# Kernel optimization log

Measured on AMD Instinct MI355X. Metric: run time of the kernel, lower is better.

## Reference

```python
import jax, jax.numpy as jnp
import numpy as np

D, H, K, L, NB = 128, 8, 16, 16, 2
N, E, MN, ME = 100_000, 800_000, 1_000, 8_000
VOCAB, BT, VP = 50_000, 256, 15
_SQD, _SQK = float(np.sqrt(D)), float(np.sqrt(K))


def _segment_softmax(score, seg, num):
    m = jax.ops.segment_max(score, seg, num_segments=num)
    e = jnp.exp(score - m[seg])
    z = jax.ops.segment_sum(e, seg, num_segments=num)
    return e / (z[seg] + 1e-9)


def _meta_learner(feat, u, W2, W1):
    # latent-attention factorization: feat [n,D] -> 2d param [n,H,K], 1d param [n,H]
    w = jax.nn.softmax((feat @ u.T) / _SQD, axis=-1)  # [n,L]
    return jnp.einsum('nl,lhk->nhk', w, W2), w @ W1


def _conv(feat, src, dst, p2n, p1n, p2e, p1e, Wq, Wk, Wv, Wo):
    # HeteroAttnConv: multi-head attention message passing modulated by
    # per-node (p2n,p1n) and per-edge (p2e,p1e) meta parameters.
    n = feat.shape[0]
    q = (feat @ Wq).reshape(n, H, K) * p2n
    kf = (feat @ Wk).reshape(n, H, K)
    v = (feat @ Wv).reshape(n, H, K)
    ke = kf[src] * p2e                                   # [e,H,K]
    score = (q[dst] * ke).sum(-1) / _SQK + p1e + p1n[dst]  # [e,H]
    attn = _segment_softmax(score, dst, n)
    agg = jax.ops.segment_sum(attn[..., None] * v[src], dst, num_segments=n).reshape(n, D)
    return jax.nn.relu(agg @ Wo), ke.reshape(-1, D)


def _forward(emb, u, W2lat, W1lat, Wq_m, Wk_m, Wv_m, Wo_m, Wq, Wk, Wv, Wo,
             node_vals, meta_node_vals, src, dst, meta_src, meta_dst,
             meta_node_id, meta_edge_id, target_idx,
             static_vals, static_src, static_dst):
    # _init_meta_param: static param-name graph, copy_u/sum then meta_learner
    fs = emb[static_vals]
    agg = jax.ops.segment_sum(fs[static_src], static_dst, num_segments=VP)
    p2s, p1s = _meta_learner(agg, u, W2lat, W1lat)
    base_tw, base_n1, base_n2 = p1s[0], p1s[3], p2s[6]   # target_weight, node 1d, node 2d
    base_e1, base_e2 = p1s[9], p2s[12]                   # edge 1d, edge 2d

    meta_feat = emb[meta_node_vals]
    feat = emb[node_vals]
    # _asign_param_to_graph(meta_graph): broadcast base buffers only
    mp2n = jnp.broadcast_to(base_n2, (MN, H, K))
    mp1n = jnp.broadcast_to(base_n1, (MN, H))
    mp2e = jnp.broadcast_to(base_e2, (ME, H, K))
    mp1e = jnp.broadcast_to(base_e1, (ME, H))

    out = jnp.zeros((BT, 1), feat.dtype)
    for b in range(NB):
        pre_meta, pre = meta_feat, feat
        meta_feat, meta_edge_feat = _conv(meta_feat, meta_src, meta_dst,
                                          mp2n, mp1n, mp2e, mp1e,
                                          Wq_m[b], Wk_m[b], Wv_m[b], Wo_m[b])
        # _asign_param_to_graph(graph, meta_node_feat, meta_edge_feat):
        # base repeat + indexed add of meta_learner outputs
        p2mn, p1mn = _meta_learner(meta_feat, u, W2lat, W1lat)
        p2me, p1me = _meta_learner(meta_edge_feat, u, W2lat, W1lat)
        p2n = base_n2[None] + p2mn[meta_node_id]
        p1n = base_n1[None] + p1mn[meta_node_id]
        tw = base_tw[None] + p1mn[meta_node_id]
        p2e = base_e2[None] + p2me[meta_edge_id]
        p1e = base_e1[None] + p1me[meta_edge_id]
        feat, _ = _conv(feat, src, dst, p2n, p1n, p2e, p1e,
                        Wq[b], Wk[b], Wv[b], Wo[b])
        # block residual
        meta_feat = meta_feat + pre_meta
        feat = feat + pre
        # Target: per-target-node weighted readout with target_weight param
        logit = jnp.einsum('th,thk->t', tw[target_idx],
                           feat[target_idx].reshape(BT, H, K))
        out = out + logit[:, None]
    return out / NB


def setup_inputs() -> dict:
    key = jax.random.key(0)
    ks = jax.random.split(key, 24)
    s = 0.05
    inp = {}
    inp['emb'] = jax.random.normal(ks[0], (VOCAB, D), jnp.float32) * s
    inp['u'] = jax.random.normal(ks[1], (L, D), jnp.float32) * s
    inp['W2lat'] = jax.random.normal(ks[2], (L, H, K), jnp.float32) * s
    inp['W1lat'] = jax.random.normal(ks[3], (L, H), jnp.float32) * s
    for i, nm in enumerate(['Wq_m', 'Wk_m', 'Wv_m', 'Wo_m', 'Wq', 'Wk', 'Wv', 'Wo']):
        inp[nm] = jax.random.normal(ks[4 + i], (NB, D, D), jnp.float32) / np.sqrt(D)
    inp['node_vals'] = jax.random.randint(ks[12], (N,), 0, VOCAB)
    inp['meta_node_vals'] = jax.random.randint(ks[13], (MN,), 0, VOCAB)
    inp['src'] = jax.random.randint(ks[14], (E,), 0, N)
    inp['dst'] = jax.random.randint(ks[15], (E,), 0, N)
    inp['meta_src'] = jax.random.randint(ks[16], (ME,), 0, MN)
    inp['meta_dst'] = jax.random.randint(ks[17], (ME,), 0, MN)
    inp['meta_node_id'] = jax.random.randint(ks[18], (N,), 0, MN)
    inp['meta_edge_id'] = jax.random.randint(ks[19], (E,), 0, ME)
    inp['target_idx'] = jax.random.randint(ks[20], (BT,), 0, N)
    # static param-name graph: 5 names x (1 name node + 2 token nodes), tokens->name
    name_pos = np.arange(5) * 3
    inp['static_vals'] = jax.random.randint(ks[21], (VP,), 0, VOCAB)
    inp['static_src'] = jnp.asarray(np.stack([name_pos + 1, name_pos + 2], 1).reshape(-1), jnp.int32)
    inp['static_dst'] = jnp.asarray(np.repeat(name_pos, 2), jnp.int32)
    return inp


def reference(emb, u, W2lat, W1lat, Wq_m, Wk_m, Wv_m, Wo_m, Wq, Wk, Wv, Wo,
              node_vals, meta_node_vals, src, dst, meta_src, meta_dst,
              meta_node_id, meta_edge_id, target_idx,
              static_vals, static_src, static_dst):
    return _forward(emb, u, W2lat, W1lat, Wq_m, Wk_m, Wv_m, Wo_m, Wq, Wk, Wv, Wo,
                    node_vals, meta_node_vals, src, dst, meta_src, meta_dst,
                    meta_node_id, meta_edge_id, target_idx,
                    static_vals, static_src, static_dst)
```

## Files before the change

kernel.cpp:

```cpp
#include <hip/hip_runtime.h>
#include <hip/hip_bf16.h>
#include <hip/hip_fp8.h>

#define DD   128
#define HH   8

typedef short bf16x8 __attribute__((ext_vector_type(8)));
typedef float f32x4  __attribute__((ext_vector_type(4)));
typedef float f32x2  __attribute__((ext_vector_type(2)));

__device__ __forceinline__ float b2f(unsigned short v){
  union { unsigned int u; float f; } x; x.u = ((unsigned int)v) << 16; return x.f;
}
__device__ __forceinline__ unsigned short f2b(float f){
  __hip_bfloat16 h = __float2bfloat16(f);
  return *(unsigned short*)&h;
}
__device__ __forceinline__ unsigned char f2f8(float x){
  __hip_fp8_e4m3 h(x);
  return h.__x;
}
__device__ __forceinline__ float f82f(unsigned char b){
  __hip_fp8_e4m3 h; h.__x = b;
  return (float)h;
}
__device__ __forceinline__ void cvt4(unsigned int w, float* o){
#if defined(__has_builtin)
# if __has_builtin(__builtin_amdgcn_cvt_pk_f32_fp8)
  f32x2 lo = __builtin_amdgcn_cvt_pk_f32_fp8((int)w, false);
  f32x2 hi = __builtin_amdgcn_cvt_pk_f32_fp8((int)w, true);
  o[0]=lo[0]; o[1]=lo[1]; o[2]=hi[0]; o[3]=hi[1];
  return;
# endif
#endif
  o[0]=f82f(w&0xff); o[1]=f82f((w>>8)&0xff);
  o[2]=f82f((w>>16)&0xff); o[3]=f82f((w>>24)&0xff);
}
struct __align__(8) us4 { unsigned short x,y,z,w; };
struct __align__(16) us8 { unsigned short s[8]; };

__device__ __forceinline__ float gld(const void* p, size_t i, bool f32){
  if (f32) return ((const float*)p)[i];
  return b2f(((const unsigned short*)p)[i]);
}

__device__ __forceinline__ void gll16(const void* g, void* l){
  __builtin_amdgcn_global_load_lds(
      (const __attribute__((address_space(1))) unsigned int*)g,
      (__attribute__((address_space(3))) unsigned int*)l, 16, 0, 0);
}

struct WPtrs { const void* p[8]; };
__global__ __launch_bounds__(256) void w_repack16(
    WPtrs W, unsigned short* __restrict__ stage, int NBt,
    const int* __restrict__ dflag)
{
  const bool wf32 = (*dflag) != 0;
  int idx = blockIdx.x >> 6;
  int ti = idx / NBt, bi = idx - ti*NBt;
  size_t bo = (size_t)bi*DD*DD;
  int i = (blockIdx.x & 63)*256 + threadIdx.x;
  int k = i >> 7, n = i & 127;
  float x;
  if (wf32) x = ((const float*)W.p[ti])[bo + i];
  else      x = b2f(((const unsigned short*)W.p[ti])[bo + i]);
  stage[(size_t)idx*DD*DD + n*DD + k] = f2b(x);
}

enum { EPI_STORE=0, EPI_SCALE_CONST=1, EPI_RELU=3,
       EPI_RELU_RES=4, EPI_RELU_RES2=5 };

#define CPAD 132


template<int EPI, bool INB, bool OUTB>
__global__ __launch_bounds__(256) void gemm128m(
    const void* __restrict__ Av, const unsigned short* __restrict__ Bt,
    void* __restrict__ Cv, int M,
    const unsigned short* __restrict__ Rb,
    const float* __restrict__ Rf, float* __restrict__ C2)
{
  __shared__ __align__(16) unsigned short Asb[64*128];
  __shared__ __align__(16) unsigned short Btb[16896];
  const int tid = threadIdx.x;
  const int wave = tid >> 6, lane = tid & 63;
  const int row0 = blockIdx.x * 64;

  if (INB){
    const char* Ab = (const char*)Av;
    int n4 = lane >> 4, c = lane & 15;
#pragma unroll
    for (int op=0; op<4; op++){
      int rA = wave*16 + op*4;
      int n = rA + n4;
      int gr = row0 + n; if (gr >= M) gr = M - 1;
      gll16(Ab + (size_t)gr*256 + ((size_t)((c ^ (n & 7)) << 4)), &Asb[rA*128]);
    }
  } else {
    const float* Af = (const float*)Av;
    int r = tid >> 2, cb = (tid & 3) * 32, rx = (r & 7) << 3;
    int gr = row0 + r;
#pragma unroll
    for (int j=0;j<8;j++){
      int cc = cb + j*4;
      float4 val = make_float4(0.f,0.f,0.f,0.f);
      if (gr < M) val = *(const float4*)(Af + (size_t)gr*DD + cc);
      us4 o; o.x=f2b(val.x); o.y=f2b(val.y); o.z=f2b(val.z); o.w=f2b(val.w);
      *(us4*)&Asb[r*128 + (cc ^ rx)] = o;
    }
  }
  {
    int n4 = lane >> 4, c = lane & 15;
#pragma unroll
    for (int op=0; op<8; op++){
      int rB = wave*32 + op*4;
      int n = rB + n4;
      gll16((const char*)Bt + (size_t)n*256 + ((size_t)((c ^ (n & 7)) << 4)),
            &Btb[rB*128]);
    }
  }
  __syncthreads();

  f32x4 acc[8];
#pragma unroll
  for (int t=0;t<8;t++) acc[t] = (f32x4){0.f,0.f,0.f,0.f};
  const int am = (lane & 15), kq = (lane >> 4) * 8, axr = (am & 7) << 3;
#pragma unroll
  for (int k0=0;k0<128;k0+=32){
    int xo = (k0 + kq) ^ axr;
    bf16x8 a = *(bf16x8*)&Asb[(wave*16 + am)*128 + xo];
#pragma unroll
    for (int t=0;t<8;t++){
      bf16x8 b = *(bf16x8*)&Btb[(t*16 + am)*128 + xo];
      acc[t] = __builtin_amdgcn_mfma_f32_16x16x32_bf16(a, b, acc[t], 0,0,0);
    }
  }
  __syncthreads();
  float* Cls = (float*)Btb;
  {
    int rr = wave*16 + (lane>>4)*4;
    int cc = lane & 15;
#pragma unroll
    for (int t=0;t<8;t++)
#pragma unroll
      for (int r=0;r<4;r++)
        Cls[(rr + r)*CPAD + t*16 + cc] = acc[t][r];
  }
  __syncthreads();

  {
    int r = tid >> 2, cb = (tid & 3) * 32;
    int gr = row0 + r;
    if (gr < M){
#pragma unroll
      for (int j=0;j<8;j++){
        int c = cb + j*4;
        float4 o = *(float4*)&Cls[r*CPAD + c];
        if (EPI == EPI_RELU_RES){
          us4 rb = *(const us4*)(Rb + (size_t)gr*DD + c);
          o.x=fmaxf(o.x,0.f)+b2f(rb.x); o.y=fmaxf(o.y,0.f)+b2f(rb.y);
          o.z=fmaxf(o.z,0.f)+b2f(rb.z); o.w=fmaxf(o.w,0.f)+b2f(rb.w);
        } else if (EPI == EPI_RELU_RES2){
          o.x=fmaxf(o.x,0.f); o.y=fmaxf(o.y,0.f); o.z=fmaxf(o.z,0.f); o.w=fmaxf(o.w,0.f);
          float4 rf = *(const float4*)(Rf + (size_t)gr*DD + c);
          *(float4*)(C2 + (size_t)gr*DD + c) =
              make_float4(o.x+rf.x, o.y+rf.y, o.z+rf.z, o.w+rf.w);
        }
        if (OUTB){
          us4 ob; ob.x=f2b(o.x); ob.y=f2b(o.y); ob.z=f2b(o.z); ob.w=f2b(o.w);
          *(us4*)((unsigned short*)Cv + (size_t)gr*DD + c) = ob;
        } else {
          *(float4*)((float*)Cv + (size_t)gr*DD + c) = o;
        }
      }
    }
  }
}

template<int EPIQ, bool INB, bool FP8KV>
__device__ __forceinline__ void qkv_body(
    unsigned short* Asb, unsigned short* Btb, int blk,
    const void* __restrict__ Av,
    const unsigned short* __restrict__ Btq, const unsigned short* __restrict__ Btk,
    const unsigned short* __restrict__ Btv,
    void* __restrict__ Cq, void* __restrict__ Ck, int stK,
    void* __restrict__ Cvo, int stV, int M,
    const float* __restrict__ svec)
{
  const int tid = threadIdx.x;
  const int wave = tid >> 6, lane = tid & 63;
  const int row0 = blk * 64;

  if (INB){
    const char* Ab = (const char*)Av;
    int n4 = lane >> 4, c = lane & 15;
#pragma unroll
    for (int op=0; op<4; op++){
      int rA = wave*16 + op*4;
      int n = rA + n4;
      int gr = row0 + n; if (gr >= M) gr = M - 1;
      gll16(Ab + (size_t)gr*256 + ((size_t)((c ^ (n & 7)) << 4)), &Asb[rA*128]);
    }
  } else {
    const float* Af = (const float*)Av;
    int r = tid >> 2, cb = (tid & 3) * 32, rx = (r & 7) << 3;
    int gr = row0 + r;
#pragma unroll
    for (int j=0;j<8;j++){
      int cc = cb + j*4;
      float4 val = make_float4(0.f,0.f,0.f,0.f);
      if (gr < M) val = *(const float4*)(Af + (size_t)gr*DD + cc);
      us4 o; o.x=f2b(val.x); o.y=f2b(val.y); o.z=f2b(val.z); o.w=f2b(val.w);
      *(us4*)&Asb[r*128 + (cc ^ rx)] = o;
    }
  }

  const unsigned short* Bts[3] = {Btq, Btk, Btv};
  void* Cs[3] = {Cq, Ck, Cvo};
  const int sts[3] = {DD, stK, stV};
  const int am = (lane & 15), kq = (lane >> 4) * 8, axr = (am & 7) << 3;

  for (int ph=0; ph<3; ph++){
    {
      const unsigned short* Bt = Bts[ph];
      int n4 = lane >> 4, c = lane & 15;
#pragma unroll
      for (int op=0; op<8; op++){
        int rB = wave*32 + op*4;
        int n = rB + n4;
        gll16((const char*)Bt + (size_t)n*256 + ((size_t)((c ^ (n & 7)) << 4)),
              &Btb[rB*128]);
      }
    }
    __syncthreads();
    f32x4 acc[8];
#pragma unroll
    for (int t=0;t<8;t++) acc[t] = (f32x4){0.f,0.f,0.f,0.f};
#pragma unroll
    for (int k0=0;k0<128;k0+=32){
      int xo = (k0 + kq) ^ axr;
      bf16x8 a = *(bf16x8*)&Asb[(wave*16 + am)*128 + xo];
#pragma unroll
      for (int t=0;t<8;t++){
        bf16x8 b = *(bf16x8*)&Btb[(t*16 + am)*128 + xo];
        acc[t] = __builtin_amdgcn_mfma_f32_16x16x32_bf16(a, b, acc[t], 0,0,0);
      }
    }
    __syncthreads();
    float* Cls = (float*)Btb;
    {
      int rr = wave*16 + (lane>>4)*4;
      int cc = lane & 15;
#pragma unroll
      for (int t=0;t<8;t++)
#pragma unroll
        for (int r=0;r<4;r++)
          Cls[(rr + r)*CPAD + t*16 + cc] = acc[t][r];
    }
    __syncthreads();
    {
      int r = tid >> 2, cb = (tid & 3) * 32;
      int gr = row0 + r;
      if (gr < M){
#pragma unroll
        for (int j=0;j<8;j++){
          int c = cb + j*4;
          float4 o = *(float4*)&Cls[r*CPAD + c];
          if (ph == 0 && EPIQ == EPI_SCALE_CONST){
            o.x*=svec[c+0]; o.y*=svec[c+1]; o.z*=svec[c+2]; o.w*=svec[c+3];
          }
          if (FP8KV && ph > 0){
            unsigned char* Cb = (unsigned char*)Cs[ph];
            uchar4 ob;
            ob.x=f2f8(o.x*8.f); ob.y=f2f8(o.y*8.f);
            ob.z=f2f8(o.z*8.f); ob.w=f2f8(o.w*8.f);
            *(uchar4*)(Cb + (size_t)gr*256 + c) = ob;
          } else {
            us4 ob; ob.x=f2b(o.x); ob.y=f2b(o.y); ob.z=f2b(o.z); ob.w=f2b(o.w);
            *(us4*)((unsigned short*)Cs[ph] + (size_t)gr*sts[ph] + c) = ob;
          }
        }
      }
    }
    __syncthreads();
  }
}

__global__ __launch_bounds__(256) void gemm_qkv2(
    const unsigned short* __restrict__ featB, const float* __restrict__ featM,
    const unsigned short* __restrict__ wqb, const unsigned short* __restrict__ wkb,
    const unsigned short* __restrict__ wvb,
    const unsigned short* __restrict__ wqm, const unsigned short* __restrict__ wkm,
    const unsigned short* __restrict__ wvm,
    unsigned short* __restrict__ qB, unsigned char* __restrict__ kv8,
    unsigned short* __restrict__ qM, unsigned short* __restrict__ kfM,
    unsigned short* __restrict__ vM,
    int Nbig, int Nmeta, int gN, const float* __restrict__ svec)
{
  __shared__ __align__(16) unsigned short Asb[64*128];
  __shared__ __align__(16) unsigned short Btb[16896];
  if (blockIdx.x < gN){
    qkv_body<EPI_STORE,true,true>(Asb, Btb, blockIdx.x, featB,
        wqb, wkb, wvb, qB, kv8, 0, kv8 + 128, 0, Nbig, svec);
  } else {
    qkv_body<EPI_SCALE_CONST,false,false>(Asb, Btb, blockIdx.x - gN, featM,
        wqm, wkm, wvm, qM, kfM, DD, vM, DD, Nmeta, svec);
  }
}

__global__ __launch_bounds__(256) void k_static(
    const void* __restrict__ emb, const int* __restrict__ svals,
    const int* __restrict__ ssrc, const int* __restrict__ sdst,
    const void* __restrict__ u, const void* __restrict__ W2,
    const void* __restrict__ W1, float* __restrict__ base, int nsrc,
    int* __restrict__ dflag)
{
  __shared__ float sagg[15][128];
  __shared__ float ssc[15][16];
  __shared__ float sww[15][16];
  __shared__ int swf;
  const int t = threadIdx.x;
  if (t < 64){
    float m = 0.f;
    for (int i=t; i<128; i+=64){
      float x = fabsf(b2f(((const unsigned short*)emb)[i]));
      if (x < 1e30f) m = fmaxf(m, x);
    }
#pragma unroll
    for (int s=1;s<64;s<<=1) m = fmaxf(m, __shfl_xor(m, s, 64));
    if (t==0){ int f = (m > 1e4f) ? 1 : 0; *dflag = f; swf = f; }
  }
  for (int i=t;i<15*128;i+=256) ((float*)sagg)[i]=0.f;
  __syncthreads();
  const bool wf32 = (swf != 0);
  if (t < 128){
    for (int i=0;i<nsrc;i++){
      int row = sdst[i]; int vr = svals[ssrc[i]];
      sagg[row][t] += gld(emb, (size_t)vr*DD + t, wf32);
    }
  }
  __syncthreads();
  if (t < 240){
    int n = t>>4, l = t&15;
    float a=0.f;
    for (int d=0;d<128;d++) a += sagg[n][d]*gld(u, l*128+d, wf32);
    ssc[n][l] = a * 0.08838834764831845f;
  }
  __syncthreads();
  if (t < 15){
    float mx=-1e30f;
    for (int l=0;l<16;l++) mx = fmaxf(mx, ssc[t][l]);
    float s=0.f;
    for (int l=0;l<16;l++){ float e=__expf(ssc[t][l]-mx); sww[t][l]=e; s+=e; }
    float inv = 1.f/s;
    for (int l=0;l<16;l++) sww[t][l]*=inv;
  }
  __syncthreads();
  if (t < 8){
    float a=0.f,b=0.f,c=0.f;
    for (int l=0;l<16;l++){
      float wv = gld(W1, l*8+t, wf32);
      a += sww[0][l]*wv; b += sww[3][l]*wv; c += sww[9][l]*wv;
    }
    base[t]=a; base[8+t]=b; base[16+t]=c;
  }
  if (t < 128){
    float a=0.f,b=0.f;
    for (int l=0;l<16;l++){
      float wv = gld(W2, l*128+t, wf32);
      a += sww[6][l]*wv; b += sww[12][l]*wv;
    }
    base[24+t]=a; base[152+t]=b;
  }
}

__global__ __launch_bounds__(256) void gather_rows2(
    const void* __restrict__ emb,
    const int* __restrict__ valsB, unsigned short* __restrict__ featB, int nB,
    const int* __restrict__ valsM, float* __restrict__ featM, int nM,
    const int* __restrict__ dflag)
{
  const bool wf32 = (*dflag) != 0;
  int i = blockIdx.x*256 + threadIdx.x;
  bool big = (i < nB*16);
  int i2 = big ? i : (i - nB*16);
  if (!big && i2 >= nM*16) return;
  int r = i2>>4, c = (i2&15)*8;
  int vr = big ? valsB[r] : valsM[r];
  float vb[8];
  if (wf32){
    float4 f0 = *(const float4*)((const float*)emb + (size_t)vr*DD + c);
    float4 f1 = *(const float4*)((const float*)emb + (size_t)vr*DD + c + 4);
    vb[0]=f0.x; vb[1]=f0.y; vb[2]=f0.z; vb[3]=f0.w;
    vb[4]=f1.x; vb[5]=f1.y; vb[6]=f1.z; vb[7]=f1.w;
  } else {
    uint4 raw = *(const uint4*)((const unsigned short*)emb + (size_t)vr*DD + c);
    const unsigned short* hw = (const unsigned short*)&raw;
#pragma unroll
    for (int j=0;j<8;j++) vb[j] = b2f(hw[j]);
  }
  if (big){
    unsigned short* d = featB + (size_t)r*DD + c;
    us4 o0, o1;
    o0.x=f2b(vb[0]); o0.y=f2b(vb[1]); o0.z=f2b(vb[2]); o0.w=f2b(vb[3]);
    o1.x=f2b(vb[4]); o1.y=f2b(vb[5]); o1.z=f2b(vb[6]); o1.w=f2b(vb[7]);
    *(us4*)d = o0; *(us4*)(d+4) = o1;
  } else {
    float* d = featM + (size_t)r*DD + c;
    *(float4*)d     = make_float4(vb[0],vb[1],vb[2],vb[3]);
    *(float4*)(d+4) = make_float4(vb[4],vb[5],vb[6],vb[7]);
  }
}

__global__ __launch_bounds__(256) void zeroi(int* __restrict__ p, int n){
  int i = blockIdx.x*256 + threadIdx.x;
  if (i < n) p[i] = 0;
}

__global__ __launch_bounds__(256) void k_hist2(
    const int* __restrict__ dstB, const int* __restrict__ dstM,
    int* __restrict__ degB, int* __restrict__ degM, int E, int ME, int nbE){
  int b = blockIdx.x, t = threadIdx.x;
  if (b < nbE){ int i = b*256+t; if (i < E) atomicAdd(&degB[dstB[i]], 1); }
  else { int i = (b-nbE)*256+t; if (i < ME) atomicAdd(&degM[dstM[i]], 1); }
}

__global__ __launch_bounds__(256) void k_scan1b(
    const int* __restrict__ degB, int* __restrict__ rpB, int* __restrict__ bsB,
    int nB, int nbB,
    const int* __restrict__ degM, int* __restrict__ rpM, int* __restrict__ bsM,
    int nM){
  __shared__ int ls[256];
  int blk = blockIdx.x, t = threadIdx.x;
  const int* deg; int* rowptr; int* bsum; int n; int b;
  if (blk < nbB){ deg=degB; rowptr=rpB; bsum=bsB; n=nB; b=blk; }
  else          { deg=degM; rowptr=rpM; bsum=bsM; n=nM; b=blk-nbB; }
  int base = b*1024 + t*4;
  int v0 = (base+0<n)?deg[base+0]:0;
  int v1 = (base+1<n)?deg[base+1]:0;
  int v2 = (base+2<n)?deg[base+2]:0;
  int v3 = (base+3<n)?deg[base+3]:0;
  int tsum = v0+v1+v2+v3;
  ls[t] = tsum; __syncthreads();
  for (int o=1;o<256;o<<=1){
    int x = (t>=o) ? ls[t-o] : 0;
    __syncthreads();
    ls[t] += x;
    __syncthreads();
  }
  int excl = ls[t]-tsum;
  if (t==255) bsum[b] = ls[255];
  if (base+0<n) rowptr[base+0]=excl;
  if (base+1<n) rowptr[base+1]=excl+v0;
  if (base+2<n) rowptr[base+2]=excl+v0+v1;
  if (base+3<n) rowptr[base+3]=excl+v0+v1+v2;
}

__global__ __launch_bounds__(256) void k_scan3b(
    int* __restrict__ rpB, const int* __restrict__ bsB, int* __restrict__ curB,
    int nB, int nb3B, int nbsB,
    int* __restrict__ rpM, const int* __restrict__ bsM, int* __restrict__ curM,
    int nM, int nbsM){
  __shared__ int spre;
  int blk = blockIdx.x, t = threadIdx.x;
  if (blk < nb3B){
    if (t == 0){
      int chunk = blk >> 2;
      int pre = 0;
      for (int j=0;j<chunk;j++) pre += bsB[j];
      spre = pre;
      if (blk == 0){
        int tot = 0;
        for (int j=0;j<nbsB;j++) tot += bsB[j];
        rpB[nB] = tot;
      }
    }
    __syncthreads();
    int i = blk*256 + t;
    if (i < nB){ int r = rpB[i] + spre; rpB[i] = r; curB[i] = r; }
  } else {
    int b2 = blk - nb3B;
    if (t == 0){
      int chunk = b2 >> 2;
      int pre = 0;
      for (int j=0;j<chunk;j++) pre += bsM[j];
      spre = pre;
      if (b2 == 0){
        int tot = 0;
        for (int j=0;j<nbsM;j++) tot += bsM[j];
        rpM[nM] = tot;
      }
    }
    __syncthreads();
    int i = b2*256 + t;
    if (i < nM){ int r = rpM[i] + spre; rpM[i] = r; curM[i] = r; }
  }
}

__global__ __launch_bounds__(256) void k_scatter2(
    const int* __restrict__ dstB, const int* __restrict__ srcB,
    const int* __restrict__ auxB, int* __restrict__ curB,
    int* __restrict__ epackB, int E, int nbE,
    const int* __restrict__ dstM, const int* __restrict__ srcM,
    int* __restrict__ curM, int* __restrict__ esrcM, int* __restrict__ eauxM,
    int ME){
  int blk = blockIdx.x, t = threadIdx.x;
  if (blk < nbE){
    int e = blk*256 + t;
    if (e < E){
      int p = atomicAdd(&curB[dstB[e]], 1);
      epackB[p] = srcB[e] | (auxB[e] << 17);
    }
  } else {
    int e = (blk-nbE)*256 + t;
    if (e < ME){
      int p = atomicAdd(&curM[dstM[e]], 1);
      esrcM[p] = srcM[e];
      eauxM[p] = e;
    }
  }
}

__global__ __launch_bounds__(256) void edge_meta_csr(
    const int* __restrict__ rowptr, const int* __restrict__ esrc,
    const int* __restrict__ eorig,
    const unsigned short* __restrict__ qm, const unsigned short* __restrict__ kfm,
    const unsigned short* __restrict__ vm,
    const float* __restrict__ base, unsigned short* __restrict__ mef,
    float* __restrict__ agg, int NM)
{
  int d = blockIdx.x*4 + (threadIdx.x>>6);
  if (d >= NM) return;
  int lane = threadIdx.x & 63;
  const float* be2 = base+152; const float* be1 = base+16; const float* bn1 = base+8;
  size_t dq = (size_t)d*DD;
  float q0 = b2f(qm[dq+lane]), q1 = b2f(qm[dq+64+lane]);
  float w0 = be2[lane], w1 = be2[64+lane];
  int h0 = lane>>4, h1 = h0+4;
  float bias0 = be1[h0] + bn1[h0];
  float bias1 = be1[h1] + bn1[h1];
  float z0=0.f, z1=0.f, a0=0.f, a1=0.f;
  int i0 = rowptr[d], i1 = rowptr[d+1];
  for (int i=i0; i<i1; i++){
    int s = esrc[i], e = eorig[i];
    size_t so=(size_t)s*DD, eo=(size_t)e*DD;
    float ke0 = b2f(kfm[so+lane])    * w0;
    float ke1 = b2f(kfm[so+64+lane]) * w1;
    mef[eo+lane]=f2b(ke0); mef[eo+64+lane]=f2b(ke1);
    float p0 = q0*ke0, p1 = q1*ke1;
#pragma unroll
    for (int m=1;m<16;m<<=1){ p0 += __shfl_xor(p0,m,64); p1 += __shfl_xor(p1,m,64); }
    float e0 = __expf(p0*0.25f + bias0);
    float e1 = __expf(p1*0.25f + bias1);
    z0 += e0; z1 += e1;
    a0 += e0*b2f(vm[so+lane]);
    a1 += e1*b2f(vm[so+64+lane]);
  }
  float inv0 = 1.f/(z0 + 1e-9f);
  float inv1 = 1.f/(z1 + 1e-9f);
  agg[dq+lane]    = a0*inv0;
  agg[dq+64+lane] = a1*inv1;
}

__global__ __launch_bounds__(128) void learner2(
    const float* __restrict__ Xa, const unsigned short* __restrict__ Xb,
    int Ma, int Mtot,
    const void* __restrict__ u, const void* __restrict__ W2,
    const void* __restrict__ W1,
    float* __restrict__ p2a, float* __restrict__ p1a,
    unsigned short* __restrict__ w2me, unsigned short* __restrict__ p1b,
    const float* __restrict__ base, const int* __restrict__ dflag)
{
  __shared__ float sX[128];
  __shared__ float st[16];
  __shared__ float sw[16];
  const bool wf32 = (*dflag) != 0;
  const int t = threadIdx.x;
  const int l = t>>3, j = t&7;
  float uc[16], w2c[16], w1c[16];
#pragma unroll
  for (int m=0;m<16;m++) uc[m] = gld(u, (size_t)l*128 + j*16 + m, wf32);
#pragma unroll
  for (int i=0;i<16;i++) w2c[i] = gld(W2, (size_t)i*128 + t, wf32);
  if (t < 8){
#pragma unroll
    for (int i=0;i<16;i++) w1c[i] = gld(W1, (size_t)i*8 + t, wf32);
  }
  for (int rr=0; rr<4; rr++){
    int row = blockIdx.x*4 + rr;
    if (row >= Mtot) break;
    const bool isB = (row >= Ma);
    const int m = isB ? (row - Ma) : row;
    if (isB) sX[t] = b2f(Xb[(size_t)m*DD + t]);
    else     sX[t] = Xa[(size_t)m*DD + t];
    __syncthreads();
    float part = 0.f;
#pragma unroll
    for (int mm=0;mm<16;mm++) part += sX[j*16+mm]*uc[mm];
    part += __shfl_xor(part,1,64); part += __shfl_xor(part,2,64); part += __shfl_xor(part,4,64);
    if (j==0) st[l] = part * 0.08838834764831845f;
    __syncthreads();
    float mx=-1e30f;
    for (int i=0;i<16;i++) mx = fmaxf(mx, st[i]);
    float ssum=0.f;
    for (int i=0;i<16;i++) ssum += __expf(st[i]-mx);
    float inv = 1.f/ssum;
    if (t<16) sw[t] = __expf(st[t]-mx)*inv;
    __syncthreads();
    float a=0.f;
#pragma unroll
    for (int i=0;i<16;i++) a += sw[i]*w2c[i];
    if (isB) w2me[(size_t)m*DD+t] = f2b(base[152+t] + a);
    else     p2a[(size_t)m*DD+t] = a;
    if (t<8){
      float bb=0.f;
#pragma unroll
      for (int i=0;i<16;i++) bb += sw[i]*w1c[i];
      if (isB) p1b[(size_t)m*HH+t] = f2b(bb);
      else     p1a[(size_t)m*HH+t] = bb;
    }
    __syncthreads();
  }
}

__global__ __launch_bounds__(256) void edge_fused(
    const int* __restrict__ rowptr, const int* __restrict__ epack,
    const int* __restrict__ mnid,
    const unsigned short* __restrict__ q, const unsigned char* __restrict__ kv8,
    const unsigned short* __restrict__ w2me, const unsigned short* __restrict__ p1me,
    const float* __restrict__ p1mn, const float* __restrict__ p2mn,
    const float* __restrict__ base,
    unsigned short* __restrict__ aggb, int N)
{
  int wv = blockIdx.x*4 + (threadIdx.x>>6);
  int lane = threadIdx.x & 63;
  int grp = lane >> 4, l16 = lane & 15;
  int d = wv*4 + grp;
  if (d >= N) return;
  int c8 = l16 * 8;
  int h = l16 >> 1;

  int i0 = rowptr[d], i1 = rowptr[d+1];
  int mn = mnid[d];
  float bias = base[16+h] + base[8+h] + p1mn[(size_t)mn*HH + h];
  size_t dq = (size_t)d*DD;
  float qv[8];
  {
    uint4 qraw = *(const uint4*)(q + dq + c8);
    const unsigned short* qh = (const unsigned short*)&qraw;
    const float* p2 = p2mn + (size_t)mn*DD + c8;
    const float* sv = base + 24 + c8;
#pragma unroll
    for (int j=0;j<8;j++) qv[j] = b2f(qh[j]) * (sv[j] + p2[j]) * 0.03125f;
  }

  float zh = 0.f;
  float a[8];
#pragma unroll
  for (int j=0;j<8;j++) a[j] = 0.f;

  int i = i0;
  for (; i + 3 < i1; i += 4){
    uint2 kr[4], vr[4]; uint4 wr[4]; float pm[4];
#pragma unroll
    for (int t=0;t<4;t++){
      unsigned int vp = (unsigned int)epack[i+t];
      int s = vp & 0x1FFFF, me = vp >> 17;
      const unsigned char* kv = kv8 + (size_t)s*256 + c8;
      kr[t] = *(const uint2*)kv;
      vr[t] = *(const uint2*)(kv + 128);
      wr[t] = *(const uint4*)(w2me + (size_t)me*DD + c8);
      pm[t] = b2f(p1me[(size_t)me*HH + h]);
    }
#pragma unroll
    for (int t=0;t<4;t++){
      float kf[8], vf[8];
      cvt4(kr[t].x, kf); cvt4(kr[t].y, kf+4);
      cvt4(vr[t].x, vf); cvt4(vr[t].y, vf+4);
      const unsigned short* wh = (const unsigned short*)&wr[t];
      float p = 0.f;
#pragma unroll
      for (int j=0;j<8;j++) p += qv[j]*(kf[j]*b2f(wh[j]));
      p += __shfl_xor(p, 1, 64);
      float ex = __expf(p + bias + pm[t]);
      zh += ex;
#pragma unroll
      for (int j=0;j<8;j++) a[j] += ex*vf[j];
    }
  }
  for (; i + 1 < i1; i += 2){
    unsigned int v0p = (unsigned int)epack[i];
    unsigned int v1p = (unsigned int)epack[i+1];
    int s0 = v0p & 0x1FFFF, me0 = v0p >> 17;
    int s1 = v1p & 0x1FFFF, me1 = v1p >> 17;
    const unsigned char* kv0 = kv8 + (size_t)s0*256 + c8;
    const unsigned char* kv1 = kv8 + (size_t)s1*256 + c8;
    uint2 kraw0 = *(const uint2*)kv0;
    uint2 vraw0 = *(const uint2*)(kv0 + 128);
    uint4 wraw0 = *(const uint4*)(w2me + (size_t)me0*DD + c8);
    float pm0 = b2f(p1me[(size_t)me0*HH + h]);
    uint2 kraw1 = *(const uint2*)kv1;
    uint2 vraw1 = *(const uint2*)(kv1 + 128);
    uint4 wraw1 = *(const uint4*)(w2me + (size_t)me1*DD + c8);
    float pm1 = b2f(p1me[(size_t)me1*HH + h]);
    float k0f[8], v0f[8], k1f[8], v1f[8];
    cvt4(kraw0.x, k0f); cvt4(kraw0.y, k0f+4);
    cvt4(vraw0.x, v0f); cvt4(vraw0.y, v0f+4);
    cvt4(kraw1.x, k1f); cvt4(kraw1.y, k1f+4);
    cvt4(vraw1.x, v1f); cvt4(vraw1.y, v1f+4);
    const unsigned short* wh0 = (const unsigned short*)&wraw0;
    const unsigned short* wh1 = (const unsigned short*)&wraw1;
    float pA = 0.f, pB = 0.f;
#pragma unroll
    for (int j=0;j<8;j++){
      pA += qv[j]*(k0f[j]*b2f(wh0[j]));
      pB += qv[j]*(k1f[j]*b2f(wh1[j]));
    }
    pA += __shfl_xor(pA, 1, 64);
    pB += __shfl_xor(pB, 1, 64);
    float ex0 = __expf(pA + bias + pm0);
    float ex1 = __expf(pB + bias + pm1);
    zh += ex0 + ex1;
#pragma unroll
    for (int j=0;j<8;j++) a[j] += ex0*v0f[j] + ex1*v1f[j];
  }
  if (i < i1){
    unsigned int vp = (unsigned int)epack[i];
    int s = vp & 0x1FFFF, me = vp >> 17;
    const unsigned char* kv = kv8 + (size_t)s*256 + c8;
    uint2 kraw = *(const uint2*)kv;
    uint2 vraw = *(const uint2*)(kv + 128);
    uint4 wraw = *(const uint4*)(w2me + (size_t)me*DD + c8);
    float pm = b2f(p1me[(size_t)me*HH + h]);
    float kf[8], vf[8];
    cvt4(kraw.x, kf); cvt4(kraw.y, kf+4);
    cvt4(vraw.x, vf); cvt4(vraw.y, vf+4);
    const unsigned short* wh = (const unsigned short*)&wraw;
    float p = 0.f;
#pragma unroll
    for (int j=0;j<8;j++) p += qv[j]*(kf[j]*b2f(wh[j]));
    p += __shfl_xor(p, 1, 64);
    float ex = __expf(p + bias + pm);
    zh += ex;
#pragma unroll
    for (int j=0;j<8;j++) a[j] += ex*vf[j];
  }

  float inv = 0.125f / (zh + 1e-9f);
  us8 o;
#pragma unroll
  for (int j=0;j<8;j++) o.s[j] = f2b(a[j]*inv);
  *(us8*)(aggb + dq + c8) = o;
}

__global__ __launch_bounds__(256) void readout(
    const int* __restrict__ tgt, const int* __restrict__ mnid,
    const unsigned short* __restrict__ featb, const float* __restrict__ p1mn,
    const float* __restrict__ base, float* __restrict__ acc,
    void* __restrict__ out, int last, float invNB, int BT,
    const int* __restrict__ dflag)
{
  int t = blockIdx.x*256 + threadIdx.x;
  int ti = t >> 4, l16 = t & 15;
  if (ti >= BT) return;
  int idx = tgt[ti]; int mn = mnid[idx];
  int h = l16 >> 1;
  float tw = base[h] + p1mn[(size_t)mn*HH + h];
  uint4 raw = *(const uint4*)(featb + (size_t)idx*DD + l16*8);
  const unsigned short* hw = (const unsigned short*)&raw;
  float s = 0.f;
#pragma unroll
  for (int j=0;j<8;j++) s += b2f(hw[j]);
  float part = tw * s;
  part += __shfl_xor(part, 1, 64);
  part += __shfl_xor(part, 2, 64);
  part += __shfl_xor(part, 4, 64);
  part += __shfl_xor(part, 8, 64);
  if (l16 == 0){
    if (!last) acc[ti] = part;
    else {
      float r = (acc[ti] + part) * invNB;
      if ((*dflag) != 0) ((float*)out)[ti] = r;
      else ((__hip_bfloat16*)out)[ti] = __float2bfloat16(r);
    }
  }
}

extern "C" void kernel_launch(void* const* d_in, const int* in_sizes, int n_in,
                              void* d_out, int out_size, void* d_ws, size_t ws_size,
                              hipStream_t stream) {
  const void* emb   = d_in[0];
  const void* u     = d_in[1];
  const void* W2lat = d_in[2];
  const void* W1lat = d_in[3];
  WPtrs wptrs;
  for (int i=0;i<8;i++) wptrs.p[i] = d_in[4+i];
  const int* node_vals      = (const int*)d_in[12];
  const int* meta_node_vals = (const int*)d_in[13];
  const int* src            = (const int*)d_in[14];
  const int* dst            = (const int*)d_in[15];
  const int* meta_src       = (const int*)d_in[16];
  const int* meta_dst       = (const int*)d_in[17];
  const int* meta_node_id   = (const int*)d_in[18];
  const int* meta_edge_id   = (const int*)d_in[19];
  const int* target_idx     = (const int*)d_in[20];
  const int* static_vals    = (const int*)d_in[21];
  const int* static_src     = (const int*)d_in[22];
  const int* static_dst     = (const int*)d_in[23];

  const int N  = in_sizes[12];
  const int MN = in_sizes[13];
  const int E  = in_sizes[14];
  const int ME = in_sizes[16];
  const int BT = in_sizes[20];
  const int NSRC = in_sizes[22];
  const int NB = in_sizes[8] / (DD*DD);

  float* ws = (float*)d_ws;
  size_t off = 0;
  auto allocf = [&](size_t n){ float* p = ws + off; off += (n + 3) & ~(size_t)3; return p; };
  auto allocb = [&](size_t n){ unsigned short* p = (unsigned short*)(ws + off); off += (((n+1)/2) + 3) & ~(size_t)3; return p; };
  auto alloci = [&](size_t n){ int* p = (int*)(ws + off); off += (n + 3) & ~(size_t)3; return p; };
  int*            dflag = (int*)ws; off += 4;
  unsigned short* feat  = allocb((size_t)N*DD);
  unsigned short* q     = allocb((size_t)N*DD);
  unsigned char*  kv8   = (unsigned char*)allocf((size_t)N*64);
  unsigned short* aggb  = allocb((size_t)N*DD);
  float*          meta_feat= allocf((size_t)MN*DD);
  float*          agg_m = allocf((size_t)MN*DD);
  unsigned short* q_m   = allocb((size_t)MN*DD);
  unsigned short* kf_m  = allocb((size_t)MN*DD);
  unsigned short* v_m   = allocb((size_t)MN*DD);
  float*          meta_out = allocf((size_t)MN*DD);
  unsigned short* mef   = allocb((size_t)ME*DD);
  float*          p2mn  = allocf((size_t)MN*DD);
  float*          p1mn  = allocf((size_t)MN*HH);
  unsigned short* w2me  = allocb((size_t)ME*DD);
  unsigned short* p1me  = allocb((size_t)ME*HH);
  float*          base  = allocf(280);
  float*          acc   = allocf((size_t)BT);
  unsigned short* wstage= allocb((size_t)8*NB*DD*DD);
  int*            rowptr= alloci((size_t)N+1);
  int*            cursor= alloci((size_t)N);
  int*            epack = alloci((size_t)E);
  int*            rowptr_m= alloci((size_t)MN+1);
  int*            cursor_m= alloci((size_t)MN);
  int*            esrc_m  = alloci((size_t)ME);
  int*            eorig_m = alloci((size_t)ME);
  int*            degAll  = alloci((size_t)(N+MN));
  int*            deg     = degAll;
  int*            deg_m   = degAll + N;
  const int nb_scan   = (N + 1023)/1024;
  const int nb_scan_m = (MN + 1023)/1024;
  int*            bsum   = alloci((size_t)nb_scan);
  int*            bsum_m = alloci((size_t)nb_scan_m);
  (void)ws_size; (void)n_in; (void)out_size;

  const float* base_n2 = base + 24;

  k_static<<<1,256,0,stream>>>(emb, static_vals, static_src, static_dst,
                               u, W2lat, W1lat, base, NSRC, dflag);
  gather_rows2<<<((N+MN)*16+255)/256,256,0,stream>>>(emb, node_vals, feat, N,
      meta_node_vals, meta_feat, MN, dflag);

  const int nbE  = (E+255)/256, nbME = (ME+255)/256;
  const int nb3B = (N+255)/256, nb3M = (MN+255)/256;
  zeroi<<<(N+MN+255)/256,256,0,stream>>>(degAll, N+MN);
  k_hist2<<<nbE+nbME,256,0,stream>>>(dst, meta_dst, deg, deg_m, E, ME, nbE);
  k_scan1b<<<nb_scan+nb_scan_m,256,0,stream>>>(deg, rowptr, bsum, N, nb_scan,
      deg_m, rowptr_m, bsum_m, MN);
  k_scan3b<<<nb3B+nb3M,256,0,stream>>>(rowptr, bsum, cursor, N, nb3B, nb_scan,
      rowptr_m, bsum_m, cursor_m, MN, nb_scan_m);
  k_scatter2<<<nbE+nbME,256,0,stream>>>(dst, src, meta_edge_id, cursor,
      epack, E, nbE, meta_dst, meta_src, cursor_m, esrc_m, eorig_m, ME);

  w_repack16<<<8*NB*64,256,0,stream>>>(wptrs, wstage, NB, dflag);

  const int gm = (MN+63)/64;
  const int gN = (N+63)/64;
  const float invNB = 1.0f/(float)NB;

  for (int b=0;b<NB;b++){
    const unsigned short* wq_m = wstage + (size_t)(0*NB+b)*DD*DD;
    const unsigned short* wk_m = wstage + (size_t)(1*NB+b)*DD*DD;
    const unsigned short* wv_m = wstage + (size_t)(2*NB+b)*DD*DD;
    const unsigned short* wo_m = wstage + (size_t)(3*NB+b)*DD*DD;
    const unsigned short* wqb  = wstage + (size_t)(4*NB+b)*DD*DD;
    const unsigned short* wkb  = wstage + (size_t)(5*NB+b)*DD*DD;
    const unsigned short* wvb  = wstage + (size_t)(6*NB+b)*DD*DD;
    const unsigned short* wob  = wstage + (size_t)(7*NB+b)*DD*DD;

    gemm_qkv2<<<gN+gm,256,0,stream>>>(feat, meta_feat,
        wqb, wkb, wvb, wq_m, wk_m, wv_m,
        q, kv8, q_m, kf_m, v_m, N, MN, gN, base_n2);

    edge_meta_csr<<<(MN+3)/4,256,0,stream>>>(rowptr_m, esrc_m, eorig_m,
        q_m, kf_m, v_m, base, mef, agg_m, MN);
    gemm128m<EPI_RELU_RES2,false,false><<<gm,256,0,stream>>>(agg_m, wo_m,
        meta_out, MN, nullptr, meta_feat, meta_feat);
    learner2<<<(MN+ME+3)/4,128,0,stream>>>(meta_out, mef, MN, MN+ME,
        u, W2lat, W1lat, p2mn, p1mn, w2me, p1me, base, dflag);

    edge_fused<<<(N+15)/16,256,0,stream>>>(rowptr, epack,
        meta_node_id, q, kv8, w2me, p1me, p1mn, p2mn, base, aggb, N);
    gemm128m<EPI_RELU_RES,true,true><<<gN,256,0,stream>>>(aggb, wob, feat, N,
        feat, nullptr, nullptr);

    readout<<<(BT*16+255)/256,256,0,stream>>>(target_idx, meta_node_id, feat, p1mn,
        base, acc, d_out, (b==NB-1) ? 1 : 0, invNB, BT, dflag);
  }
}
```

Measured before the change: 571.9 us.

## Fuse readout into output GEMM epilogue and merge init/repack kernels

The per-block readout kernel is removed. The target-weighted row sum is now computed in the epilogue of the node output GEMM and atomically added to the accumulator, using a target-to-row linked list built in the scatter kernel. The weight repack is merged into the gather kernel, and the zero-init also resets the accumulators, which cuts several launches. The 4-edge unrolled loop in edge_fused is also dropped, leaving the 2-edge loop. Atomic float adds change the summation order slightly, and removing the wider unroll may reduce memory-level parallelism in the edge kernel.

Measured after the change: 554.7 us. -3.0%, faster.

```diff
diff --git a/kernel.cpp b/kernel.cpp
--- a/kernel.cpp
+++ b/kernel.cpp
@@ -51,34 +51,22 @@
 }
 
 struct WPtrs { const void* p[8]; };
-__global__ __launch_bounds__(256) void w_repack16(
-    WPtrs W, unsigned short* __restrict__ stage, int NBt,
-    const int* __restrict__ dflag)
-{
-  const bool wf32 = (*dflag) != 0;
-  int idx = blockIdx.x >> 6;
-  int ti = idx / NBt, bi = idx - ti*NBt;
-  size_t bo = (size_t)bi*DD*DD;
-  int i = (blockIdx.x & 63)*256 + threadIdx.x;
-  int k = i >> 7, n = i & 127;
-  float x;
-  if (wf32) x = ((const float*)W.p[ti])[bo + i];
-  else      x = b2f(((const unsigned short*)W.p[ti])[bo + i]);
-  stage[(size_t)idx*DD*DD + n*DD + k] = f2b(x);
-}
 
 enum { EPI_STORE=0, EPI_SCALE_CONST=1, EPI_RELU=3,
        EPI_RELU_RES=4, EPI_RELU_RES2=5 };
 
 #define CPAD 132
-
 
 template<int EPI, bool INB, bool OUTB>
 __global__ __launch_bounds__(256) void gemm128m(
     const void* __restrict__ Av, const unsigned short* __restrict__ Bt,
     void* __restrict__ Cv, int M,
     const unsigned short* __restrict__ Rb,
-    const float* __restrict__ Rf, float* __restrict__ C2)
+    const float* __restrict__ Rf, float* __restrict__ C2,
+    const int* __restrict__ mnid, const float* __restrict__ p1mn,
+    const float* __restrict__ base,
+    const int* __restrict__ tgt_of, const int* __restrict__ tgt_next,
+    float* __restrict__ acc)
 {
   __shared__ __align__(16) unsigned short Asb[64*128];
   __shared__ __align__(16) unsigned short Btb[16896];
@@ -121,9 +109,9 @@
   }
   __syncthreads();
 
-  f32x4 acc[8];
-#pragma unroll
-  for (int t=0;t<8;t++) acc[t] = (f32x4){0.f,0.f,0.f,0.f};
+  f32x4 acc0[8];
+#pragma unroll
+  for (int t=0;t<8;t++) acc0[t] = (f32x4){0.f,0.f,0.f,0.f};
   const int am = (lane & 15), kq = (lane >> 4) * 8, axr = (am & 7) << 3;
 #pragma unroll
   for (int k0=0;k0<128;k0+=32){
@@ -132,7 +120,7 @@
 #pragma unroll
     for (int t=0;t<8;t++){
       bf16x8 b = *(bf16x8*)&Btb[(t*16 + am)*128 + xo];
-      acc[t] = __builtin_amdgcn_mfma_f32_16x16x32_bf16(a, b, acc[t], 0,0,0);
+      acc0[t] = __builtin_amdgcn_mfma_f32_16x16x32_bf16(a, b, acc0[t], 0,0,0);
     }
   }
   __syncthreads();
@@ -144,7 +132,7 @@
     for (int t=0;t<8;t++)
 #pragma unroll
       for (int r=0;r<4;r++)
-        Cls[(rr + r)*CPAD + t*16 + cc] = acc[t][r];
+        Cls[(rr + r)*CPAD + t*16 + cc] = acc0[t][r];
   }
   __syncthreads();
 
@@ -152,6 +140,7 @@
     int r = tid >> 2, cb = (tid & 3) * 32;
     int gr = row0 + r;
     if (gr < M){
+      float hs0 = 0.f, hs1 = 0.f;
 #pragma unroll
       for (int j=0;j<8;j++){
         int c = cb + j*4;
@@ -160,6 +149,8 @@
           us4 rb = *(const us4*)(Rb + (size_t)gr*DD + c);
           o.x=fmaxf(o.x,0.f)+b2f(rb.x); o.y=fmaxf(o.y,0.f)+b2f(rb.y);
           o.z=fmaxf(o.z,0.f)+b2f(rb.z); o.w=fmaxf(o.w,0.f)+b2f(rb.w);
+          float s4 = o.x + o.y + o.z + o.w;
+          if (j < 4) hs0 += s4; else hs1 += s4;
         } else if (EPI == EPI_RELU_RES2){
           o.x=fmaxf(o.x,0.f); o.y=fmaxf(o.y,0.f); o.z=fmaxf(o.z,0.f); o.w=fmaxf(o.w,0.f);
           float4 rf = *(const float4*)(Rf + (size_t)gr*DD + c);
@@ -171,6 +162,22 @@
           *(us4*)((unsigned short*)Cv + (size_t)gr*DD + c) = ob;
         } else {
           *(float4*)((float*)Cv + (size_t)gr*DD + c) = o;
+        }
+      }
+      if (EPI == EPI_RELU_RES){
+        int hb = cb >> 4;
+        int mn = mnid[gr];
+        float tw0 = base[hb]     + p1mn[(size_t)mn*HH + hb];
+        float tw1 = base[hb + 1] + p1mn[(size_t)mn*HH + hb + 1];
+        float part = tw0*hs0 + tw1*hs1;
+        part += __shfl_xor(part, 1, 64);
+        part += __shfl_xor(part, 2, 64);
+        if ((tid & 3) == 0){
+          int ti = tgt_of[gr];
+          while (ti >= 0){
+            atomicAdd(&acc[ti], part);
+            ti = tgt_next[ti];
+          }
         }
       }
     }
@@ -374,13 +381,27 @@
   }
 }
 
-__global__ __launch_bounds__(256) void gather_rows2(
+__global__ __launch_bounds__(256) void gather_repack(
     const void* __restrict__ emb,
     const int* __restrict__ valsB, unsigned short* __restrict__ featB, int nB,
     const int* __restrict__ valsM, float* __restrict__ featM, int nM,
-    const int* __restrict__ dflag)
+    WPtrs W, unsigned short* __restrict__ stage, int NBt,
+    const int* __restrict__ dflag, int gB)
 {
   const bool wf32 = (*dflag) != 0;
+  if ((int)blockIdx.x >= gB){
+    int bid = blockIdx.x - gB;
+    int idx = bid >> 6;
+    int ti = idx / NBt, bi = idx - ti*NBt;
+    size_t bo = (size_t)bi*DD*DD;
+    int i = (bid & 63)*256 + threadIdx.x;
+    int k = i >> 7, n = i & 127;
+    float x;
+    if (wf32) x = ((const float*)W.p[ti])[bo + i];
+    else      x = b2f(((const unsigned short*)W.p[ti])[bo + i]);
+    stage[(size_t)idx*DD*DD + n*DD + k] = f2b(x);
+    return;
+  }
   int i = blockIdx.x*256 + threadIdx.x;
   bool big = (i < nB*16);
   int i2 = big ? i : (i - nB*16);
@@ -412,9 +433,15 @@
   }
 }
 
-__global__ __launch_bounds__(256) void zeroi(int* __restrict__ p, int n){
+__global__ __launch_bounds__(256) void k_init(
+    int* __restrict__ degAll, int nDeg,
+    int* __restrict__ tgt_of, int Nn,
+    float* __restrict__ acc, int BT)
+{
   int i = blockIdx.x*256 + threadIdx.x;
-  if (i < n) p[i] = 0;
+  if (i < nDeg) degAll[i] = 0;
+  if (i < Nn) tgt_of[i] = -1;
+  if (i < BT) acc[i] = 0.f;
 }
 
 __global__ __launch_bounds__(256) void k_hist2(
@@ -503,7 +530,9 @@
     int* __restrict__ epackB, int E, int nbE,
     const int* __restrict__ dstM, const int* __restrict__ srcM,
     int* __restrict__ curM, int* __restrict__ esrcM, int* __restrict__ eauxM,
-    int ME){
+    int ME, int nbME,
+    const int* __restrict__ tgt, int* __restrict__ tgt_of,
+    int* __restrict__ tgt_next, int BT){
   int blk = blockIdx.x, t = threadIdx.x;
   if (blk < nbE){
     int e = blk*256 + t;
@@ -511,12 +540,17 @@
       int p = atomicAdd(&curB[dstB[e]], 1);
       epackB[p] = srcB[e] | (auxB[e] << 17);
     }
-  } else {
+  } else if (blk < nbE + nbME){
     int e = (blk-nbE)*256 + t;
     if (e < ME){
       int p = atomicAdd(&curM[dstM[e]], 1);
       esrcM[p] = srcM[e];
       eauxM[p] = e;
+    }
+  } else {
+    for (int i=t; i<BT; i+=256){
+      int old = atomicExch(&tgt_of[tgt[i]], i);
+      tgt_next[i] = old;
     }
   }
 }
@@ -660,34 +694,6 @@
   for (int j=0;j<8;j++) a[j] = 0.f;
 
   int i = i0;
-  for (; i + 3 < i1; i += 4){
-    uint2 kr[4], vr[4]; uint4 wr[4]; float pm[4];
-#pragma unroll
-    for (int t=0;t<4;t++){
-      unsigned int vp = (unsigned int)epack[i+t];
-      int s = vp & 0x1FFFF, me = vp >> 17;
-      const unsigned char* kv = kv8 + (size_t)s*256 + c8;
-      kr[t] = *(const uint2*)kv;
-      vr[t] = *(const uint2*)(kv + 128);
-      wr[t] = *(const uint4*)(w2me + (size_t)me*DD + c8);
-      pm[t] = b2f(p1me[(size_t)me*HH + h]);
-    }
-#pragma unroll
-    for (int t=0;t<4;t++){
-      float kf[8], vf[8];
-      cvt4(kr[t].x, kf); cvt4(kr[t].y, kf+4);
-      cvt4(vr[t].x, vf); cvt4(vr[t].y, vf+4);
-      const unsigned short* wh = (const unsigned short*)&wr[t];
-      float p = 0.f;
-#pragma unroll
-      for (int j=0;j<8;j++) p += qv[j]*(kf[j]*b2f(wh[j]));
-      p += __shfl_xor(p, 1, 64);
-      float ex = __expf(p + bias + pm[t]);
-      zh += ex;
-#pragma unroll
-      for (int j=0;j<8;j++) a[j] += ex*vf[j];
-    }
-  }
   for (; i + 1 < i1; i += 2){
     unsigned int v0p = (unsigned int)epack[i];
     unsigned int v1p = (unsigned int)epack[i+1];
@@ -753,37 +759,15 @@
   *(us8*)(aggb + dq + c8) = o;
 }
 
-__global__ __launch_bounds__(256) void readout(
-    const int* __restrict__ tgt, const int* __restrict__ mnid,
-    const unsigned short* __restrict__ featb, const float* __restrict__ p1mn,
-    const float* __restrict__ base, float* __restrict__ acc,
-    void* __restrict__ out, int last, float invNB, int BT,
-    const int* __restrict__ dflag)
+__global__ __launch_bounds__(256) void k_finish(
+    const float* __restrict__ acc, void* __restrict__ out,
+    float invNB, int BT, const int* __restrict__ dflag)
 {
   int t = blockIdx.x*256 + threadIdx.x;
-  int ti = t >> 4, l16 = t & 15;
-  if (ti >= BT) return;
-  int idx = tgt[ti]; int mn = mnid[idx];
-  int h = l16 >> 1;
-  float tw = base[h] + p1mn[(size_t)mn*HH + h];
-  uint4 raw = *(const uint4*)(featb + (size_t)idx*DD + l16*8);
-  const unsigned short* hw = (const unsigned short*)&raw;
-  float s = 0.f;
-#pragma unroll
-  for (int j=0;j<8;j++) s += b2f(hw[j]);
-  float part = tw * s;
-  part += __shfl_xor(part, 1, 64);
-  part += __shfl_xor(part, 2, 64);
-  part += __shfl_xor(part, 4, 64);
-  part += __shfl_xor(part, 8, 64);
-  if (l16 == 0){
-    if (!last) acc[ti] = part;
-    else {
-      float r = (acc[ti] + part) * invNB;
-      if ((*dflag) != 0) ((float*)out)[ti] = r;
-      else ((__hip_bfloat16*)out)[ti] = __float2bfloat16(r);
-    }
-  }
+  if (t >= BT) return;
+  float r = acc[t] * invNB;
+  if ((*dflag) != 0) ((float*)out)[t] = r;
+  else ((__hip_bfloat16*)out)[t] = __float2bfloat16(r);
 }
 
 extern "C" void kernel_launch(void* const* d_in, const int* in_sizes, int n_in,
@@ -850,6 +834,8 @@
   int*            degAll  = alloci((size_t)(N+MN));
   int*            deg     = degAll;
   int*            deg_m   = degAll + N;
+  int*            tgt_of  = alloci((size_t)N);
+  int*            tgt_next= alloci((size_t)BT);
   const int nb_scan   = (N + 1023)/1024;
   const int nb_scan_m = (MN + 1023)/1024;
   int*            bsum   = alloci((size_t)nb_scan);
@@ -858,23 +844,23 @@
 
   const float* base_n2 = base + 24;
 
+  k_init<<<(N+MN+255)/256,256,0,stream>>>(degAll, N+MN, tgt_of, N, acc, BT);
   k_static<<<1,256,0,stream>>>(emb, static_vals, static_src, static_dst,
                                u, W2lat, W1lat, base, NSRC, dflag);
-  gather_rows2<<<((N+MN)*16+255)/256,256,0,stream>>>(emb, node_vals, feat, N,
-      meta_node_vals, meta_feat, MN, dflag);
+  const int gB = ((N+MN)*16+255)/256;
+  gather_repack<<<gB + 8*NB*64,256,0,stream>>>(emb, node_vals, feat, N,
+      meta_node_vals, meta_feat, MN, wptrs, wstage, NB, dflag, gB);
 
   const int nbE  = (E+255)/256, nbME = (ME+255)/256;
   const int nb3B = (N+255)/256, nb3M = (MN+255)/256;
-  zeroi<<<(N+MN+255)/256,256,0,stream>>>(degAll, N+MN);
   k_hist2<<<nbE+nbME,256,0,stream>>>(dst, meta_dst, deg, deg_m, E, ME, nbE);
   k_scan1b<<<nb_scan+nb_scan_m,256,0,stream>>>(deg, rowptr, bsum, N, nb_scan,
       deg_m, rowptr_m, bsum_m, MN);
   k_scan3b<<<nb3B+nb3M,256,0,stream>>>(rowptr, bsum, cursor, N, nb3B, nb_scan,
       rowptr_m, bsum_m, cursor_m, MN, nb_scan_m);
-  k_scatter2<<<nbE+nbME,256,0,stream>>>(dst, src, meta_edge_id, cursor,
-      epack, E, nbE, meta_dst, meta_src, cursor_m, esrc_m, eorig_m, ME);
-
-  w_repack16<<<8*NB*64,256,0,stream>>>(wptrs, wstage, NB, dflag);
+  k_scatter2<<<nbE+nbME+1,256,0,stream>>>(dst, src, meta_edge_id, cursor,
+      epack, E, nbE, meta_dst, meta_src, cursor_m, esrc_m, eorig_m, ME, nbME,
+      target_idx, tgt_of, tgt_next, BT);
 
   const int gm = (MN+63)/64;
   const int gN = (N+63)/64;
@@ -897,16 +883,16 @@
     edge_meta_csr<<<(MN+3)/4,256,0,stream>>>(rowptr_m, esrc_m, eorig_m,
         q_m, kf_m, v_m, base, mef, agg_m, MN);
     gemm128m<EPI_RELU_RES2,false,false><<<gm,256,0,stream>>>(agg_m, wo_m,
-        meta_out, MN, nullptr, meta_feat, meta_feat);
+        meta_out, MN, nullptr, meta_feat, meta_feat,
+        nullptr, nullptr, nullptr, nullptr, nullptr, nullptr);
     learner2<<<(MN+ME+3)/4,128,0,stream>>>(meta_out, mef, MN, MN+ME,
         u, W2lat, W1lat, p2mn, p1mn, w2me, p1me, base, dflag);
 
     edge_fused<<<(N+15)/16,256,0,stream>>>(rowptr, epack,
         meta_node_id, q, kv8, w2me, p1me, p1mn, p2mn, base, aggb, N);
     gemm128m<EPI_RELU_RES,true,true><<<gN,256,0,stream>>>(aggb, wob, feat, N,
-        feat, nullptr, nullptr);
-
-    readout<<<(BT*16+255)/256,256,0,stream>>>(target_idx, meta_node_id, feat, p1mn,
-        base, acc, d_out, (b==NB-1) ? 1 : 0, invNB, BT, dflag);
-  }
-}
+        feat, nullptr, nullptr,
+        meta_node_id, p1mn, base, tgt_of, tgt_next, acc);
+  }
+  k_finish<<<(BT+255)/256,256,0,stream>>>(acc, d_out, invNB, BT, dflag);
+}
```
